# Performance work log

Measured on AMD Instinct MI355X. Metric: run time of the kernel, lower is better.

## Reference

```python
import jax, jax.numpy as jnp
import numpy as np
from jax import lax

LRELU_SLOPE = 0.2
EPS = 1e-8


def _modconv(x, w_style, weight, mod_w, mod_b, demodulate, upsample):
    """Per-sample modulated conv, expressed as input-scale + shared conv + output demod.

    Mathematically identical to conv2d(x, (W*s)*d, groups=B):
      conv(x_b, d_b * s_b * W) == d_b * conv(x_b * s_b, W)  (conv is linear).
    x: [B,Cin,H,W], weight: [Cout,Cin,k,k], mod_w: [Cin,S], mod_b: [Cin].
    """
    B = x.shape[0]
    s = w_style @ mod_w.T + mod_b                      # [B, Cin]
    xs = x * s[:, :, None, None]
    if upsample:
        Bn, C, H, W = xs.shape
        # torch F.interpolate(scale_factor=2, mode='bilinear', align_corners=False)
        xs = jax.image.resize(xs, (Bn, C, 2 * H, 2 * W), method='bilinear')
    k = weight.shape[-1]
    pad = k // 2
    out = lax.conv_general_dilated(
        xs, weight, window_strides=(1, 1), padding=[(pad, pad), (pad, pad)],
        dimension_numbers=('NCHW', 'OIHW', 'NCHW'))
    if demodulate:
        wmod = weight[None] * s[:, None, :, None, None]            # [B,Cout,Cin,k,k]
        d = lax.rsqrt(jnp.sum(wmod * wmod, axis=(2, 3, 4)) + EPS)  # [B,Cout]
        out = out * d[:, :, None, None]
    return out


def _leaky(x):
    return jnp.where(x >= 0, x, LRELU_SLOPE * x)


def setup_inputs() -> dict:
    key = jax.random.key(0)
    ks = jax.random.split(key, 16)
    B, Cin, Cout, S, H, W = 8, 512, 512, 512, 32, 32
    Ho, Wo = 2 * H, 2 * W
    return {
        'x': jax.random.normal(ks[0], (B, Cin, H, W), jnp.float32),
        'w': jax.random.normal(ks[1], (B, S), jnp.float32),
        'conv1_weight': jax.random.normal(ks[2], (Cout, Cin, 3, 3), jnp.float32),
        'mod1_w': jax.random.normal(ks[3], (Cin, S), jnp.float32) * 0.02,
        'mod1_b': jnp.ones((Cin,), jnp.float32),
        'noise_scale1': jax.random.normal(ks[4], (Cout,), jnp.float32) * 0.1,
        'conv2_weight': jax.random.normal(ks[5], (Cout, Cout, 3, 3), jnp.float32),
        'mod2_w': jax.random.normal(ks[6], (Cout, S), jnp.float32) * 0.02,
        'mod2_b': jnp.ones((Cout,), jnp.float32),
        'noise_scale2': jax.random.normal(ks[7], (Cout,), jnp.float32) * 0.1,
        'rgb_weight': jax.random.normal(ks[8], (3, Cout, 1, 1), jnp.float32),
        'modr_w': jax.random.normal(ks[9], (Cout, S), jnp.float32) * 0.02,
        'modr_b': jnp.ones((Cout,), jnp.float32),
        'noise1': jax.random.normal(ks[10], (B, 1, Ho, Wo), jnp.float32),
        'noise2': jax.random.normal(ks[11], (B, 1, Ho, Wo), jnp.float32),
    }


def reference(x, w, conv1_weight, mod1_w, mod1_b, noise_scale1,
              conv2_weight, mod2_w, mod2_b, noise_scale2,
              rgb_weight, modr_w, modr_b, noise1, noise2):
    h = _modconv(x, w, conv1_weight, mod1_w, mod1_b, demodulate=True, upsample=True)
    h = _leaky(h + noise_scale1[None, :, None, None] * noise1)
    h = _modconv(h, w, conv2_weight, mod2_w, mod2_b, demodulate=True, upsample=False)
    h = _leaky(h + noise_scale2[None, :, None, None] * noise2)
    rgb = _modconv(h, w, rgb_weight, modr_w, modr_b, demodulate=False, upsample=False)
    return (h, rgb)
```

## Files before the change

kernel.cpp:

```cpp
#include <hip/hip_runtime.h>

#define LRELU 0.2f
#define EPS_D 1e-8f

static constexpr int B = 8;
static constexpr int C = 512;
static constexpr int HO = 64, WO = 64;
static constexpr int HW = HO * WO;
static constexpr int HIN = 32;

typedef _Float16 f16;
typedef _Float16 f16x8 __attribute__((ext_vector_type(8)));
typedef _Float16 f16x4 __attribute__((ext_vector_type(4)));
typedef float f32x4 __attribute__((ext_vector_type(4)));

static constexpr size_t XUP_B  = 0;
static constexpr size_t H1S_B  = 33554432;
static constexpr size_t WP1_B  = 67108864;
static constexpr size_t WP2_B  = 71827456;
static constexpr size_t S1_B   = 76546048;
static constexpr size_t S2_B   = S1_B + 16384;
static constexpr size_t SR_B   = S2_B + 16384;
static constexpr size_t D1_B   = SR_B + 16384;
static constexpr size_t D2_B   = D1_B + 16384;
static constexpr size_t WSQ1_B = D2_B + 16384;
static constexpr size_t WSQ2_B = WSQ1_B + 1048576;

__global__ void k_styles3(const float* __restrict__ wsty,
                          const float* __restrict__ mw0, const float* __restrict__ mb0, float* __restrict__ so0,
                          const float* __restrict__ mw1, const float* __restrict__ mb1, float* __restrict__ so1,
                          const float* __restrict__ mw2, const float* __restrict__ mb2, float* __restrict__ so2) {
  __shared__ float wsh[C];
  int b = blockIdx.x;
  int which = blockIdx.y;
  const float* mw = which == 0 ? mw0 : (which == 1 ? mw1 : mw2);
  const float* mb = which == 0 ? mb0 : (which == 1 ? mb1 : mb2);
  float* sout     = which == 0 ? so0 : (which == 1 ? so1 : so2);
  int t = threadIdx.x;
  wsh[t]       = wsty[b * C + t];
  wsh[t + 256] = wsty[b * C + t + 256];
  __syncthreads();
  for (int i = t; i < C; i += 256) {
    float acc = mb[i];
    const float* row = mw + (size_t)i * C;
#pragma unroll 4
    for (int j = 0; j < C; ++j) acc = fmaf(wsh[j], row[j], acc);
    sout[b * C + i] = acc;
  }
}

__global__ void k_packw(const float* __restrict__ w, f16* __restrict__ wp,
                        float* __restrict__ wsq) {
  int idx = blockIdx.x * 256 + threadIdx.x;
  const float* src = w + (size_t)idx * 9;
  float acc = 0.f;
#pragma unroll
  for (int tap = 0; tap < 9; ++tap) {
    float v = src[tap];
    wp[(size_t)tap * (C * C) + idx] = (f16)v;
    acc = fmaf(v, v, acc);
  }
  wsq[idx] = acc;
}

__global__ void k_demod(const float* __restrict__ wsq,
                        const float* __restrict__ s,
                        float* __restrict__ dout) {
  __shared__ float ssq[B * C];
  __shared__ float red[4][B];
  int co = blockIdx.x;
  int t = threadIdx.x;
  for (int idx = t; idx < B * C; idx += 256) {
    float v = s[idx];
    ssq[idx] = v * v;
  }
  __syncthreads();
  int ci0 = t * 2;
  float w0 = wsq[(size_t)co * C + ci0];
  float w1 = wsq[(size_t)co * C + ci0 + 1];
  float p[B];
#pragma unroll
  for (int b = 0; b < B; ++b) {
    p[b] = fmaf(ssq[b * C + ci0], w0, ssq[b * C + ci0 + 1] * w1);
  }
  int lane = t & 63, wv = t >> 6;
#pragma unroll
  for (int b = 0; b < B; ++b) {
    float v = p[b];
    for (int off = 32; off; off >>= 1) v += __shfl_down(v, off);
    if (lane == 0) red[wv][b] = v;
  }
  __syncthreads();
  if (t < B) {
    float tot = red[0][t] + red[1][t] + red[2][t] + red[3][t];
    dout[t * C + co] = rsqrtf(tot + EPS_D);
  }
}

__device__ __forceinline__ void up1d(int o, int& i0, int& i1, float& w0, float& w1) {
  float src = 0.5f * (float)o - 0.25f;
  float f = floorf(src);
  float fr = src - f;
  int i = (int)f;
  i0 = i < 0 ? 0 : i;
  int j = i + 1;
  i1 = j > (HIN - 1) ? (HIN - 1) : j;
  w1 = fr;
  w0 = 1.0f - fr;
}

__global__ __launch_bounds__(256) void k_up(const float* __restrict__ x,
                                            const float* __restrict__ s1,
                                            f16* __restrict__ xup) {
  __shared__ f16 xt[10 * 32 * 32];
  int bx = blockIdx.x;
  int b = bx >> 6;
  int ci0 = ((bx >> 2) & 15) * 32;
  int q = bx & 3;
  int ybase = q * 8 - 1;
  int t = threadIdx.x;
  int xi_ = t & 31, cl = t >> 5;
  for (int yl = 0; yl < 10; ++yl) {
    int y = ybase + yl;
    y = y < 0 ? 0 : (y > 31 ? 31 : y);
#pragma unroll
    for (int p = 0; p < 4; ++p) {
      int ci = p * 8 + cl;
      xt[(yl * 32 + xi_) * 32 + ci] =
          (f16)x[(((size_t)b * C + ci0 + ci) * 32 + y) * 32 + xi_];
    }
  }
  __syncthreads();
  int xo = t >> 2;
  int cg = (t & 3) * 8;
  float sv[8];
#pragma unroll
  for (int e = 0; e < 8; ++e) sv[e] = s1[b * C + ci0 + cg + e];
  int x0, x1; float wx0, wx1;
  up1d(xo, x0, x1, wx0, wx1);
  for (int yy = 0; yy < 16; ++yy) {
    int yo = q * 16 + yy;
    int y0, y1; float wy0, wy1;
    up1d(yo, y0, y1, wy0, wy1);
    int yl0 = y0 - ybase, yl1 = y1 - ybase;
    f16x8 t00 = *(const f16x8*)&xt[(yl0 * 32 + x0) * 32 + cg];
    f16x8 t01 = *(const f16x8*)&xt[(yl0 * 32 + x1) * 32 + cg];
    f16x8 t10 = *(const f16x8*)&xt[(yl1 * 32 + x0) * 32 + cg];
    f16x8 t11 = *(const f16x8*)&xt[(yl1 * 32 + x1) * 32 + cg];
    f16x8 o;
#pragma unroll
    for (int e = 0; e < 8; ++e) {
      float v = wy0 * (wx0 * (float)t00[e] + wx1 * (float)t01[e]) +
                wy1 * (wx0 * (float)t10[e] + wx1 * (float)t11[e]);
      o[e] = (f16)(v * sv[e]);
    }
    *(f16x8*)&xup[(((size_t)b * 64 + yo) * 64 + xo) * C + ci0 + cg] = o;
  }
}

__global__ __launch_bounds__(256, 2) void k_conv_mfma(
    const f16* __restrict__ xin,
    const f16* __restrict__ Wp,
    const float* __restrict__ dmod,
    const float* __restrict__ nscale,
    const float* __restrict__ noise,
    const float* __restrict__ s2v,
    f16* __restrict__ out_nhwc,
    float* __restrict__ out_nchw) {
  __shared__ char xsb[4 * 6336];
  __shared__ char wsb3[12 * 2112];

  int bx = blockIdx.x;
  int b = bx >> 6;
  int rem = bx & 63;
  int co_base = (rem >> 4) * 128;
  int y0 = (rem & 15) * 4;
  int t = threadIdx.x;
  int lane = t & 63, wid = t >> 6;
  int ln = lane & 15, kg = lane >> 4;

  f32x4 acc[8][4] = {};

  for (int ck = 0; ck < 16; ++ck) {
    for (int dyg = 0; dyg < 3; ++dyg) {
      __syncthreads();
      if (dyg == 0) {
        for (int idx = t; idx < 1584; idx += 256) {
          int c2 = idx & 3;
          int pc = idx >> 2;
          int row = pc / 66, col = pc - row * 66;
          int gy = y0 + row - 1, gx = col - 1;
          f16x8 v = {};
          if ((unsigned)gy < 64u && (unsigned)gx < 64u)
            v = *(const f16x8*)&xin[(((size_t)b * 64 + gy) * 64 + gx) * C + ck * 32 + c2 * 8];
          *(f16x8*)(xsb + c2 * 6336 + pc * 16) = v;
        }
      }
#pragma unroll
      for (int i = 0; i < 6; ++i) {
        int idx = i * 256 + t;
        int c2 = idx & 3;
        int co = (idx >> 2) & 127;
        int dx = idx >> 9;
        f16x8 v = *(const f16x8*)&Wp[((size_t)((dyg * 3 + dx) * C) + co_base + co) * C + ck * 32 + c2 * 8];
        *(f16x8*)(wsb3 + (dx * 4 + c2) * 2112 + co * 16) = v;
      }
      __syncthreads();

#pragma unroll
      for (int dx = 0; dx < 3; ++dx) {
        f16x8 af[8], bf[4];
#pragma unroll
        for (int m = 0; m < 8; ++m)
          af[m] = *(const f16x8*)(wsb3 + (dx * 4 + kg) * 2112 + (m * 16 + ln) * 16);
        int pcb = (wid + dyg) * 66 + ln + dx;
#pragma unroll
        for (int n = 0; n < 4; ++n)
          bf[n] = *(const f16x8*)(xsb + kg * 6336 + (pcb + n * 16) * 16);
#pragma unroll
        for (int m = 0; m < 8; ++m)
#pragma unroll
          for (int n = 0; n < 4; ++n)
            acc[m][n] = __builtin_amdgcn_mfma_f32_16x16x32_f16(af[m], bf[n], acc[m][n], 0, 0, 0);
      }
    }
  }

  int yo = y0 + wid;
  float nz[4];
#pragma unroll
  for (int n = 0; n < 4; ++n) nz[n] = noise[b * HW + yo * 64 + n * 16 + ln];

  if (out_nhwc) {
#pragma unroll
    for (int m = 0; m < 8; ++m) {
      int cog = co_base + m * 16 + kg * 4;
      f32x4 d4 = *(const f32x4*)&dmod[b * C + cog];
      f32x4 n4 = *(const f32x4*)&nscale[cog];
      f32x4 s4 = *(const f32x4*)&s2v[b * C + cog];
#pragma unroll
      for (int n = 0; n < 4; ++n) {
        int xo = n * 16 + ln;
        f16x4 o;
#pragma unroll
        for (int r = 0; r < 4; ++r) {
          float v = fmaf(acc[m][n][r], d4[r], n4[r] * nz[n]);
          v = v >= 0.f ? v : LRELU * v;
          o[r] = (f16)(v * s4[r]);
        }
        *(f16x4*)&out_nhwc[(((size_t)b * 64 + yo) * 64 + xo) * C + cog] = o;
      }
    }
  } else {
#pragma unroll
    for (int m = 0; m < 8; ++m) {
      int cog = co_base + m * 16 + kg * 4;
      f32x4 d4 = *(const f32x4*)&dmod[b * C + cog];
      f32x4 n4 = *(const f32x4*)&nscale[cog];
#pragma unroll
      for (int n = 0; n < 4; ++n) {
        int xo = n * 16 + ln;
#pragma unroll
        for (int r = 0; r < 4; ++r) {
          float v = fmaf(acc[m][n][r], d4[r], n4[r] * nz[n]);
          v = v >= 0.f ? v : LRELU * v;
          out_nchw[(((size_t)b * C + cog + r) * 64 + yo) * 64 + xo] = v;
        }
      }
    }
  }
}

__global__ void k_rgb(const float* __restrict__ h,
                      const float* __restrict__ rw,
                      const float* __restrict__ sr,
                      float* __restrict__ rgb) {
  __shared__ float wsr[3][C];
  int bx = blockIdx.x;
  int b = bx >> 4;
  int chunk = bx & 15;
  int t = threadIdx.x;
  for (int idx = t; idx < 3 * C; idx += 256) {
    int c = idx >> 9, co = idx & 511;
    wsr[c][co] = rw[c * C + co] * sr[b * C + co];
  }
  __syncthreads();
  int px = chunk * 256 + t;
  float a0 = 0.f, a1 = 0.f, a2 = 0.f;
  const float* hp = h + (size_t)b * C * HW + px;
#pragma unroll 4
  for (int co = 0; co < C; ++co) {
    float hv = hp[(size_t)co * HW];
    a0 = fmaf(wsr[0][co], hv, a0);
    a1 = fmaf(wsr[1][co], hv, a1);
    a2 = fmaf(wsr[2][co], hv, a2);
  }
  float* rp = rgb + (size_t)b * 3 * HW + px;
  rp[0] = a0;
  rp[HW] = a1;
  rp[2 * HW] = a2;
}

extern "C" void kernel_launch(void* const* d_in, const int* in_sizes, int n_in,
                              void* d_out, int out_size, void* d_ws, size_t ws_size,
                              hipStream_t stream) {
  (void)in_sizes; (void)n_in; (void)out_size; (void)ws_size;
  const float* x   = (const float*)d_in[0];
  const float* wst = (const float*)d_in[1];
  const float* w1  = (const float*)d_in[2];
  const float* m1w = (const float*)d_in[3];
  const float* m1b = (const float*)d_in[4];
  const float* ns1 = (const float*)d_in[5];
  const float* w2  = (const float*)d_in[6];
  const float* m2w = (const float*)d_in[7];
  const float* m2b = (const float*)d_in[8];
  const float* ns2 = (const float*)d_in[9];
  const float* rw  = (const float*)d_in[10];
  const float* mrw = (const float*)d_in[11];
  const float* mrb = (const float*)d_in[12];
  const float* nz1 = (const float*)d_in[13];
  const float* nz2 = (const float*)d_in[14];

  char* wsb = (char*)d_ws;
  f16*   xup  = (f16*)(wsb + XUP_B);
  f16*   h1s  = (f16*)(wsb + H1S_B);
  f16*   wp1  = (f16*)(wsb + WP1_B);
  f16*   wp2  = (f16*)(wsb + WP2_B);
  float* s1   = (float*)(wsb + S1_B);
  float* s2   = (float*)(wsb + S2_B);
  float* srr  = (float*)(wsb + SR_B);
  float* dm1  = (float*)(wsb + D1_B);
  float* dm2  = (float*)(wsb + D2_B);
  float* wsq1 = (float*)(wsb + WSQ1_B);
  float* wsq2 = (float*)(wsb + WSQ2_B);

  float* hout   = (float*)d_out;
  float* rgbout = hout + (size_t)B * C * HW;

  k_styles3<<<dim3(B, 3), 256, 0, stream>>>(wst, m1w, m1b, s1, m2w, m2b, s2, mrw, mrb, srr);
  k_packw<<<C * C / 256, 256, 0, stream>>>(w1, wp1, wsq1);
  k_packw<<<C * C / 256, 256, 0, stream>>>(w2, wp2, wsq2);
  k_demod<<<C, 256, 0, stream>>>(wsq1, s1, dm1);
  k_demod<<<C, 256, 0, stream>>>(wsq2, s2, dm2);
  k_up<<<B * 64, 256, 0, stream>>>(x, s1, xup);
  k_conv_mfma<<<512, 256, 0, stream>>>(xup, wp1, dm1, ns1, nz1, s2, h1s, nullptr);
  k_conv_mfma<<<512, 256, 0, stream>>>(h1s, wp2, dm2, ns2, nz2, nullptr, nullptr, hout);
  k_rgb<<<B * 16, 256, 0, stream>>>(hout, rw, srr, rgbout);
}
```

Measured before the change: 506.8 us.

## Split small kernels across more blocks, coalesce weight packing, and pad LDS strides

Four separate changes. The style GEMV and the RGB 1x1 conv now split their reduction dimension across two half-blocks and combine the halves through shared memory, and both launch with more blocks to fill more CUs. The weight-pack kernel stages its input through shared memory so the global reads are coalesced. The LDS row strides in the MFMA conv are padded (6336→6368, 2112→2144) to change the bank mapping of the fragment loads, at the cost of a slightly larger shared-memory footprint per block.

```diff
diff --git a/kernel.cpp b/kernel.cpp
--- a/kernel.cpp
+++ b/kernel.cpp
@@ -13,6 +13,9 @@
 typedef _Float16 f16x8 __attribute__((ext_vector_type(8)));
 typedef _Float16 f16x4 __attribute__((ext_vector_type(4)));
 typedef float f32x4 __attribute__((ext_vector_type(4)));
+
+static constexpr int XSS = 6368;
+static constexpr int WSS = 2144;
 
 static constexpr size_t XUP_B  = 0;
 static constexpr size_t H1S_B  = 33554432;
@@ -31,8 +34,10 @@
                           const float* __restrict__ mw1, const float* __restrict__ mb1, float* __restrict__ so1,
                           const float* __restrict__ mw2, const float* __restrict__ mb2, float* __restrict__ so2) {
   __shared__ float wsh[C];
+  __shared__ float red[128];
   int b = blockIdx.x;
   int which = blockIdx.y;
+  int slice = blockIdx.z;
   const float* mw = which == 0 ? mw0 : (which == 1 ? mw1 : mw2);
   const float* mb = which == 0 ? mb0 : (which == 1 ? mb1 : mb2);
   float* sout     = which == 0 ? so0 : (which == 1 ? so1 : so2);
@@ -40,27 +45,35 @@
   wsh[t]       = wsty[b * C + t];
   wsh[t + 256] = wsty[b * C + t + 256];
   __syncthreads();
-  for (int i = t; i < C; i += 256) {
-    float acc = mb[i];
-    const float* row = mw + (size_t)i * C;
+  int i = slice * 128 + (t & 127);
+  int jh = t >> 7;
+  const float* row = mw + (size_t)i * C + jh * 256;
+  const float* wp = wsh + jh * 256;
+  float acc = 0.f;
 #pragma unroll 4
-    for (int j = 0; j < C; ++j) acc = fmaf(wsh[j], row[j], acc);
-    sout[b * C + i] = acc;
-  }
+  for (int j = 0; j < 256; ++j) acc = fmaf(wp[j], row[j], acc);
+  if (t >= 128) red[t - 128] = acc;
+  __syncthreads();
+  if (t < 128) sout[b * C + i] = acc + red[t] + mb[i];
 }
 
 __global__ void k_packw(const float* __restrict__ w, f16* __restrict__ wp,
                         float* __restrict__ wsq) {
-  int idx = blockIdx.x * 256 + threadIdx.x;
-  const float* src = w + (size_t)idx * 9;
+  __shared__ float buf[2304];
+  int t = threadIdx.x;
+  size_t base = (size_t)blockIdx.x * 2304;
+  for (int i = t; i < 2304; i += 256) buf[i] = w[base + i];
+  __syncthreads();
+  int idx0 = blockIdx.x * 256;
+  const float* src = buf + t * 9;
   float acc = 0.f;
 #pragma unroll
   for (int tap = 0; tap < 9; ++tap) {
     float v = src[tap];
-    wp[(size_t)tap * (C * C) + idx] = (f16)v;
+    wp[(size_t)tap * (C * C) + idx0 + t] = (f16)v;
     acc = fmaf(v, v, acc);
   }
-  wsq[idx] = acc;
+  wsq[idx0 + t] = acc;
 }
 
 __global__ void k_demod(const float* __restrict__ wsq,
@@ -167,8 +180,8 @@
     const float* __restrict__ s2v,
     f16* __restrict__ out_nhwc,
     float* __restrict__ out_nchw) {
-  __shared__ char xsb[4 * 6336];
-  __shared__ char wsb3[12 * 2112];
+  __shared__ char xsb[4 * XSS];
+  __shared__ char wsb3[12 * WSS];
 
   int bx = blockIdx.x;
   int b = bx >> 6;
@@ -193,7 +206,7 @@
           f16x8 v = {};
           if ((unsigned)gy < 64u && (unsigned)gx < 64u)
             v = *(const f16x8*)&xin[(((size_t)b * 64 + gy) * 64 + gx) * C + ck * 32 + c2 * 8];
-          *(f16x8*)(xsb + c2 * 6336 + pc * 16) = v;
+          *(f16x8*)(xsb + c2 * XSS + pc * 16) = v;
         }
       }
 #pragma unroll
@@ -203,7 +216,7 @@
         int co = (idx >> 2) & 127;
         int dx = idx >> 9;
         f16x8 v = *(const f16x8*)&Wp[((size_t)((dyg * 3 + dx) * C) + co_base + co) * C + ck * 32 + c2 * 8];
-        *(f16x8*)(wsb3 + (dx * 4 + c2) * 2112 + co * 16) = v;
+        *(f16x8*)(wsb3 + (dx * 4 + c2) * WSS + co * 16) = v;
       }
       __syncthreads();
 
@@ -212,11 +225,11 @@
         f16x8 af[8], bf[4];
 #pragma unroll
         for (int m = 0; m < 8; ++m)
-          af[m] = *(const f16x8*)(wsb3 + (dx * 4 + kg) * 2112 + (m * 16 + ln) * 16);
+          af[m] = *(const f16x8*)(wsb3 + (dx * 4 + kg) * WSS + (m * 16 + ln) * 16);
         int pcb = (wid + dyg) * 66 + ln + dx;
 #pragma unroll
         for (int n = 0; n < 4; ++n)
-          bf[n] = *(const f16x8*)(xsb + kg * 6336 + (pcb + n * 16) * 16);
+          bf[n] = *(const f16x8*)(xsb + kg * XSS + (pcb + n * 16) * 16);
 #pragma unroll
         for (int m = 0; m < 8; ++m)
 #pragma unroll
@@ -276,29 +289,37 @@
                       const float* __restrict__ sr,
                       float* __restrict__ rgb) {
   __shared__ float wsr[3][C];
+  __shared__ float red[3][128];
   int bx = blockIdx.x;
-  int b = bx >> 4;
-  int chunk = bx & 15;
+  int b = bx >> 5;
+  int chunk = bx & 31;
   int t = threadIdx.x;
   for (int idx = t; idx < 3 * C; idx += 256) {
     int c = idx >> 9, co = idx & 511;
     wsr[c][co] = rw[c * C + co] * sr[b * C + co];
   }
   __syncthreads();
-  int px = chunk * 256 + t;
+  int px = chunk * 128 + (t & 127);
+  int co0 = (t >> 7) * 256;
   float a0 = 0.f, a1 = 0.f, a2 = 0.f;
-  const float* hp = h + (size_t)b * C * HW + px;
+  const float* hp = h + ((size_t)b * C + co0) * HW + px;
 #pragma unroll 4
-  for (int co = 0; co < C; ++co) {
+  for (int co = 0; co < 256; ++co) {
     float hv = hp[(size_t)co * HW];
-    a0 = fmaf(wsr[0][co], hv, a0);
-    a1 = fmaf(wsr[1][co], hv, a1);
-    a2 = fmaf(wsr[2][co], hv, a2);
-  }
-  float* rp = rgb + (size_t)b * 3 * HW + px;
-  rp[0] = a0;
-  rp[HW] = a1;
-  rp[2 * HW] = a2;
+    a0 = fmaf(wsr[0][co0 + co], hv, a0);
+    a1 = fmaf(wsr[1][co0 + co], hv, a1);
+    a2 = fmaf(wsr[2][co0 + co], hv, a2);
+  }
+  if (t >= 128) {
+    red[0][t - 128] = a0; red[1][t - 128] = a1; red[2][t - 128] = a2;
+  }
+  __syncthreads();
+  if (t < 128) {
+    float* rp = rgb + (size_t)b * 3 * HW + px;
+    rp[0]      = a0 + red[0][t];
+    rp[HW]     = a1 + red[1][t];
+    rp[2 * HW] = a2 + red[2][t];
+  }
 }
 
 extern "C" void kernel_launch(void* const* d_in, const int* in_sizes, int n_in,
@@ -337,7 +358,7 @@
   float* hout   = (float*)d_out;
   float* rgbout = hout + (size_t)B * C * HW;
 
-  k_styles3<<<dim3(B, 3), 256, 0, stream>>>(wst, m1w, m1b, s1, m2w, m2b, s2, mrw, mrb, srr);
+  k_styles3<<<dim3(B, 3, 4), 256, 0, stream>>>(wst, m1w, m1b, s1, m2w, m2b, s2, mrw, mrb, srr);
   k_packw<<<C * C / 256, 256, 0, stream>>>(w1, wp1, wsq1);
   k_packw<<<C * C / 256, 256, 0, stream>>>(w2, wp2, wsq2);
   k_demod<<<C, 256, 0, stream>>>(wsq1, s1, dm1);
@@ -345,5 +366,5 @@
   k_up<<<B * 64, 256, 0, stream>>>(x, s1, xup);
   k_conv_mfma<<<512, 256, 0, stream>>>(xup, wp1, dm1, ns1, nz1, s2, h1s, nullptr);
   k_conv_mfma<<<512, 256, 0, stream>>>(h1s, wp2, dm2, ns2, nz2, nullptr, nullptr, hout);
-  k_rgb<<<B * 16, 256, 0, stream>>>(hout, rw, srr, rgbout);
-}
+  k_rgb<<<B * 32, 256, 0, stream>>>(hout, rw, srr, rgbout);
+}
```

Result: faster. 470.0 us (-7.3%).
